# Kernel optimization log

Hardware: AMD Instinct MI355X
Metric: run time of the kernel (lower is better)

The kernel has to match this reference:

```python
import jax, jax.numpy as jnp
import numpy as np

DT = 0.02
Z_DIM = 32
U_DIM = 16


def _mlp(x, layers):
    # layers: list of (W, b); SiLU between all but last layer
    n = len(layers)
    for i, (W, b) in enumerate(layers):
        x = x @ W + b
        if i < n - 1:
            x = jax.nn.silu(x)
    return x


def _forward(x, u,
             e_w1, e_b1, e_w2, e_b2, e_w3, e_b3,
             d_w1, d_b1, d_w2, d_b2, d_w3, d_b3, d_w4, d_b4,
             a_w1, a_b1, a_w2, a_b2, a_w3, a_b3,
             b_w1, b_b1, b_w2, b_b2, b_w3, b_b3):
    # encode
    z = _mlp(x, [(e_w1, e_b1), (e_w2, e_b2), (e_w3, e_b3)])          # (B, Z)
    # state-dependent A(x) parameters: pairs (a_i, b_i) per 2x2 block
    aux = _mlp(x, [(a_w1, a_b1), (a_w2, a_b2), (a_w3, a_b3)])        # (B, Z)
    a = aux[:, 0::2]                                                  # (B, Z/2)
    b = aux[:, 1::2]
    f = jnp.exp(a * DT)
    c = jnp.cos(b * DT)
    s = jnp.sin(b * DT)
    # A(x) @ z without materializing block-diagonal: per-pair rotation-scale
    z0 = z[:, 0::2]
    z1 = z[:, 1::2]
    Az = jnp.stack([f * (c * z0 - s * z1), f * (s * z0 + c * z1)], axis=-1).reshape(z.shape)
    # B(x) @ u
    Bmat = _mlp(x, [(b_w1, b_b1), (b_w2, b_b2), (b_w3, b_b3)]).reshape(-1, Z_DIM, U_DIM)
    Bu = jnp.einsum('bzu,bu->bz', Bmat, u)
    # latent Euler step + decode
    z_next = z + DT * (Az + Bu)
    return _mlp(z_next, [(d_w1, d_b1), (d_w2, d_b2), (d_w3, d_b3), (d_w4, d_b4)])


def setup_inputs() -> dict:
    key = jax.random.key(0)
    ks = iter(jax.random.split(key, 32))
    def w(shape, scale=0.02):
        return jax.random.normal(next(ks), shape, jnp.float32) * scale
    B, X, U, Z, H, A = 16384, 64, 16, 32, 1024, 256
    return {
        'x': jax.random.normal(next(ks), (B, X), jnp.float32),
        'u': jax.random.normal(next(ks), (B, U), jnp.float32),
        'e_w1': w((X, H)), 'e_b1': w((H,)),
        'e_w2': w((H, H)), 'e_b2': w((H,)),
        'e_w3': w((H, Z)), 'e_b3': w((Z,)),
        'd_w1': w((Z, H)), 'd_b1': w((H,)),
        'd_w2': w((H, H)), 'd_b2': w((H,)),
        'd_w3': w((H, H)), 'd_b3': w((H,)),
        'd_w4': w((H, X)), 'd_b4': w((X,)),
        'a_w1': w((X, A)), 'a_b1': w((A,)),
        'a_w2': w((A, A)), 'a_b2': w((A,)),
        'a_w3': w((A, Z)), 'a_b3': w((Z,)),
        'b_w1': w((X, A)), 'b_b1': w((A,)),
        'b_w2': w((A, A)), 'b_b2': w((A,)),
        'b_w3': w((A, Z * U)), 'b_b3': w((Z * U,)),
    }


def reference(x, u,
              e_w1, e_b1, e_w2, e_b2, e_w3, e_b3,
              d_w1, d_b1, d_w2, d_b2, d_w3, d_b3, d_w4, d_b4,
              a_w1, a_b1, a_w2, a_b2, a_w3, a_b3,
              b_w1, b_b1, b_w2, b_b2, b_w3, b_b3):
    return _forward(x, u,
                    e_w1, e_b1, e_w2, e_b2, e_w3, e_b3,
                    d_w1, d_b1, d_w2, d_b2, d_w3, d_b3, d_w4, d_b4,
                    a_w1, a_b1, a_w2, a_b2, a_w3, a_b3,
                    b_w1, b_b1, b_w2, b_b2, b_w3, b_b3)
```

## Files before the change

kernel.cpp:

```cpp
#include <hip/hip_runtime.h>
#include <cstdint>
#include <cstddef>

#define B_SZ 16384
#define X_D  64
#define U_D  16
#define Z_D  32
#define H_D  1024
#define A_D  256
#define DT_C 0.02f

typedef _Float16 f16;
typedef f16   f16x8 __attribute__((ext_vector_type(8)));
typedef f16   f16x4 __attribute__((ext_vector_type(4)));
typedef float f32x4 __attribute__((ext_vector_type(4)));
typedef float f32x16 __attribute__((ext_vector_type(16)));

#define AS1 __attribute__((address_space(1)))
#define AS3 __attribute__((address_space(3)))

__device__ __forceinline__ void gld_lds16(const void* g, void* l) {
    __builtin_amdgcn_global_load_lds((AS1 void*)(g), (AS3 void*)(l), 16, 0, 0);
}

struct GArg {
    const f16*  A;
    const f16*  W;
    const float* bias;
    void*       C;
    int lda, ldc, K;
};
struct GSet { GArg g[3]; int yn0, yn1; };

template<int BM,int BN,int BK,int WM,int WN,bool SILU,int OM>
__launch_bounds__(256)
__global__ void gemm_k(GSet p)
{
    static_assert(OM != 1 || BN == 128, "OM1 repack assumes BN=128");
    int yb = blockIdx.y, gi = 0;
    if (yb >= p.yn0) { yb -= p.yn0; gi = 1; if (yb >= p.yn1) { yb -= p.yn1; gi = 2; } }
    const GArg ga = p.g[gi];

    constexpr int SEGROW = BK / 8;
    constexpr int SMASK  = (SEGROW < 8 ? SEGROW : 8) - 1;
    constexpr int WTM = BM / WM, WTN = BN / WN;
    static_assert(WTM % 32 == 0 && WTN % 32 == 0, "wave tile in 32x32 units");
    constexpr int RM = WTM / 32, RN = WTN / 32;
    constexpr int KS = BK / 16;
    constexpr int ITA = (BM * SEGROW) / 256;
    constexpr int ITB = (BN * SEGROW) / 256;

    constexpr int STAGE_B = (BM + BN) * BK * 2;
    constexpr int CS_B    = (OM == 1) ? BM * BN * 2 : 0;
    constexpr int SMEM_B  = STAGE_B > CS_B ? STAGE_B : CS_B;
    __shared__ __align__(16) char smem[SMEM_B];
    f16* As = (f16*)smem;
    f16* Bs = As + BM * BK;

    const int tid  = threadIdx.x;
    const int lane = tid & 63;
    const int wave = tid >> 6;
    const int wm = wave / WN, wn = wave % WN;
    const int l31 = lane & 31, half = lane >> 5;

    const size_t arow0 = (size_t)blockIdx.x * BM;
    const size_t brow0 = (size_t)yb * BN;
    const int lda = ga.lda, K = ga.K;

    const f16* aptr[ITA];
    const f16* bptr[ITB];
#pragma unroll
    for (int it = 0; it < ITA; ++it) {
        int s = it * 256 + tid;
        int row = s / SEGROW, st = s % SEGROW;
        int sg = st ^ (row & SMASK);
        aptr[it] = ga.A + (arow0 + row) * lda + sg * 8;
    }
#pragma unroll
    for (int it = 0; it < ITB; ++it) {
        int s = it * 256 + tid;
        int row = s / SEGROW, st = s % SEGROW;
        int sg = st ^ (row & SMASK);
        bptr[it] = ga.W + (brow0 + row) * K + sg * 8;
    }

    f32x16 acc[RM][RN];
#pragma unroll
    for (int i = 0; i < RM; ++i)
#pragma unroll
        for (int j = 0; j < RN; ++j)
#pragma unroll
            for (int r = 0; r < 16; ++r) acc[i][j][r] = 0.f;

    for (int k0 = 0; k0 < K; k0 += BK) {
#pragma unroll
        for (int it = 0; it < ITA; ++it) {
            gld_lds16(aptr[it], &As[(it * 256 + tid) * 8]);
            aptr[it] += BK;
        }
#pragma unroll
        for (int it = 0; it < ITB; ++it) {
            gld_lds16(bptr[it], &Bs[(it * 256 + tid) * 8]);
            bptr[it] += BK;
        }
        __syncthreads();

#pragma unroll
        for (int ks = 0; ks < KS; ++ks) {
            f16x8 af[RM], bf[RN];
#pragma unroll
            for (int i = 0; i < RM; ++i) {
                int row = wm * WTM + i * 32 + l31;
                int st  = (ks * 2 + half) ^ (row & SMASK);
                af[i] = *(const f16x8*)&As[(row * SEGROW + st) * 8];
            }
#pragma unroll
            for (int j = 0; j < RN; ++j) {
                int row = wn * WTN + j * 32 + l31;
                int st  = (ks * 2 + half) ^ (row & SMASK);
                bf[j] = *(const f16x8*)&Bs[(row * SEGROW + st) * 8];
            }
#pragma unroll
            for (int i = 0; i < RM; ++i)
#pragma unroll
                for (int j = 0; j < RN; ++j)
                    acc[i][j] = __builtin_amdgcn_mfma_f32_32x32x16_f16(
                        af[i], bf[j], acc[i][j], 0, 0, 0);
        }
        __syncthreads();
    }

    const int rowbL = wm * WTM;
    const int colbL = wn * WTN;

    if constexpr (OM == 1) {
        f16* Cs = (f16*)smem;
#pragma unroll
        for (int j = 0; j < RN; ++j) {
            int colL = colbL + j * 32 + l31;
            float bv = ga.bias[(int)brow0 + colL];
            int chL = colL >> 3, wi = colL & 7;
#pragma unroll
            for (int i = 0; i < RM; ++i) {
#pragma unroll
                for (int r = 0; r < 16; ++r) {
                    int rowL = rowbL + i * 32 + (r & 3) + 8 * (r >> 2) + 4 * half;
                    float v = acc[i][j][r] + bv;
                    if (SILU) v = v / (1.0f + __expf(-v));
                    Cs[rowL * BN + ((chL ^ (rowL & 15)) << 3) + wi] = (f16)v;
                }
            }
        }
        __syncthreads();
        f16* Cout = (f16*)ga.C;
#pragma unroll
        for (int pass = 0; pass < (BM * BN / 8) / 256; ++pass) {
            int s = pass * 256 + tid;
            int rowL = s >> 4;
            int ch = s & 15;
            f16x8 v = *(const f16x8*)&Cs[rowL * BN + ((ch ^ (rowL & 15)) << 3)];
            *(f16x8*)&Cout[(size_t)(arow0 + rowL) * ga.ldc + brow0 + ch * 8] = v;
        }
    } else {
        float* Cout = (float*)ga.C;
#pragma unroll
        for (int j = 0; j < RN; ++j) {
            int col = (int)brow0 + colbL + j * 32 + l31;
            float bv = ga.bias[col];
#pragma unroll
            for (int i = 0; i < RM; ++i) {
#pragma unroll
                for (int r = 0; r < 16; ++r) {
                    int row = (int)arow0 + rowbL + i * 32
                            + (r & 3) + 8 * (r >> 2) + 4 * half;
                    float v = acc[i][j][r] + bv;
                    if (SILU) v = v / (1.0f + __expf(-v));
                    Cout[(size_t)row * ga.ldc + col] = v;
                }
            }
        }
    }
}

__launch_bounds__(256)
__global__ void mid_k(const f16* __restrict__ cc2,
                      const f16* __restrict__ e_w3t, const float* __restrict__ e_b3,
                      const f16* __restrict__ a_w3t, const float* __restrict__ a_b3,
                      const f16* __restrict__ b_w3t, const float* __restrict__ b_b3,
                      const float* __restrict__ u,   f16* __restrict__ znb)
{
    __shared__ __align__(16) f16 As[32 * 64];
    __shared__ __align__(16) f16 Bs[128 * 64];
    __shared__ float zb[32 * 32];
    __shared__ float ab[32 * 32];
    __shared__ float bu[32 * 32];
    __shared__ float ub[32 * 16];

    const int tid  = threadIdx.x;
    const int lane = tid & 63, wave = tid >> 6;
    const int l15 = lane & 15, quad = lane >> 4;
    const int r0 = blockIdx.x * 32;

    ub[tid]       = u[r0 * 16 + tid];
    ub[tid + 256] = u[r0 * 16 + 256 + tid];

#pragma unroll 1
    for (int ph = 0; ph < 2; ++ph) {
        const f16* W    = ph ? a_w3t : e_w3t;
        const float* bs = ph ? a_b3 : e_b3;
        const int K     = ph ? 256 : 1024;
        const int co    = ph ? 1024 : 0;
        float* ob       = ph ? ab : zb;
        f32x4 acc = {0.f, 0.f, 0.f, 0.f};
        for (int k0 = 0; k0 < K; k0 += 64) {
            {
                int row = tid >> 3, sg = (tid & 7) ^ (row & 7);
                gld_lds16(cc2 + (size_t)(r0 + row) * 1536 + co + k0 + sg * 8,
                          &As[tid * 8]);
            }
            {
                int row = tid >> 3, sg = (tid & 7) ^ (row & 7);
                gld_lds16(W + (size_t)row * K + k0 + sg * 8, &Bs[tid * 8]);
            }
            __syncthreads();
#pragma unroll
            for (int kk = 0; kk < 64; kk += 32) {
                int ar = ((wave >> 1) << 4) + l15;
                int ast = ((kk >> 3) + quad) ^ (ar & 7);
                f16x8 af = *(const f16x8*)&As[(ar * 8 + ast) * 8];
                int br = ((wave & 1) << 4) + l15;
                int bst = ((kk >> 3) + quad) ^ (br & 7);
                f16x8 bf = *(const f16x8*)&Bs[(br * 8 + bst) * 8];
                acc = __builtin_amdgcn_mfma_f32_16x16x32_f16(af, bf, acc, 0, 0, 0);
            }
            __syncthreads();
        }
#pragma unroll
        for (int r = 0; r < 4; ++r) {
            int row = ((wave >> 1) << 4) + quad * 4 + r;
            int col = ((wave & 1) << 4) + l15;
            ob[row * 32 + col] = acc[r] + bs[col];
        }
    }

#pragma unroll 1
    for (int ch = 0; ch < 4; ++ch) {
        f32x4 acc[2][2];
#pragma unroll
        for (int i = 0; i < 2; ++i)
#pragma unroll
            for (int j = 0; j < 2; ++j) acc[i][j] = f32x4{0.f, 0.f, 0.f, 0.f};
        for (int k0 = 0; k0 < 256; k0 += 64) {
            {   int row = tid >> 3, sg = (tid & 7) ^ (row & 7);
                gld_lds16(cc2 + (size_t)(r0 + row) * 1536 + 1280 + k0 + sg * 8,
                          &As[tid * 8]);
            }
#pragma unroll
            for (int it = 0; it < 4; ++it) {
                int s = it * 256 + tid;
                int row = s >> 3, sg = (s & 7) ^ (row & 7);
                gld_lds16(b_w3t + (size_t)(ch * 128 + row) * 256 + k0 + sg * 8,
                          &Bs[s * 8]);
            }
            __syncthreads();
#pragma unroll
            for (int kk = 0; kk < 64; kk += 32) {
                f16x8 af[2], bf[2];
#pragma unroll
                for (int i = 0; i < 2; ++i) {
                    int ar = i * 16 + l15;
                    int st = ((kk >> 3) + quad) ^ (ar & 7);
                    af[i] = *(const f16x8*)&As[(ar * 8 + st) * 8];
                }
#pragma unroll
                for (int j = 0; j < 2; ++j) {
                    int br = wave * 32 + j * 16 + l15;
                    int st = ((kk >> 3) + quad) ^ (br & 7);
                    bf[j] = *(const f16x8*)&Bs[(br * 8 + st) * 8];
                }
#pragma unroll
                for (int i = 0; i < 2; ++i)
#pragma unroll
                    for (int j = 0; j < 2; ++j)
                        acc[i][j] = __builtin_amdgcn_mfma_f32_16x16x32_f16(
                            af[i], bf[j], acc[i][j], 0, 0, 0);
            }
            __syncthreads();
        }
#pragma unroll
        for (int j = 0; j < 2; ++j) {
            int colg = ch * 128 + wave * 32 + j * 16 + l15;
            float bv = b_b3[colg];
            int z = colg >> 4;
#pragma unroll
            for (int i = 0; i < 2; ++i) {
#pragma unroll
                for (int r = 0; r < 4; ++r) {
                    int row = i * 16 + quad * 4 + r;
                    float v = (acc[i][j][r] + bv) * ub[row * 16 + l15];
                    v += __shfl_xor(v, 8, 16);
                    v += __shfl_xor(v, 4, 16);
                    v += __shfl_xor(v, 2, 16);
                    v += __shfl_xor(v, 1, 16);
                    if (l15 == 0) bu[row * 32 + z] = v;
                }
            }
        }
    }
    __syncthreads();

#pragma unroll
    for (int t = 0; t < 4; ++t) {
        int idx = t * 256 + tid;
        int row = idx >> 5, z = idx & 31;
        int pb = idx & ~1;
        float a  = ab[pb], b = ab[pb + 1];
        float z0 = zb[pb], z1 = zb[pb + 1];
        float f  = __expf(a * DT_C);
        float c_ = __cosf(b * DT_C);
        float s_ = __sinf(b * DT_C);
        float Az = (z & 1) ? f * (s_ * z0 + c_ * z1) : f * (c_ * z0 - s_ * z1);
        float zc = (z & 1) ? z1 : z0;
        znb[(size_t)(r0 + row) * 32 + z] = (f16)(zc + DT_C * (Az + bu[idx]));
    }
}

struct PrepArgs {
    const float* w[13];
    f16*         wt[13];
    int          K[13];
    int          N[13];
    const float* bsrc[3];
    float*       bias1;
    const float* x;
    f16*         xb;
};

__launch_bounds__(256)
__global__ void prep_k(PrepArgs pa, int ntrans, int ncvt)
{
    int bid = blockIdx.x;
    if (bid < ntrans) {
        int i = 0, t;
        for (;; ++i) {
            t = (pa.K[i] >> 5) * (pa.N[i] >> 5);
            if (bid < t) break;
            bid -= t;
        }
        const int K = pa.K[i], N = pa.N[i];
        const int tn = N >> 5;
        const int k0 = (bid / tn) << 5, n0 = (bid % tn) << 5;
        __shared__ float tbuf[32][33];
        const int tx = threadIdx.x & 31, ty = threadIdx.x >> 5;
        const float* src = pa.w[i];
        f16* dst = pa.wt[i];
#pragma unroll
        for (int r = 0; r < 32; r += 8)
            tbuf[ty + r][tx] = src[(size_t)(k0 + ty + r) * N + n0 + tx];
        __syncthreads();
#pragma unroll
        for (int r = 0; r < 32; r += 8)
            dst[(size_t)(n0 + ty + r) * K + k0 + tx] = (f16)tbuf[tx][ty + r];
    } else if (bid < ntrans + ncvt) {
        int i = ((bid - ntrans) * 256 + threadIdx.x) * 4;
        float4 v = *(const float4*)(pa.x + i);
        f16x4 o = {(f16)v.x, (f16)v.y, (f16)v.z, (f16)v.w};
        *(f16x4*)(pa.xb + i) = o;
    } else {
        int idx = (bid - ntrans - ncvt) * 256 + (int)threadIdx.x;
        float v = (idx < 1024) ? pa.bsrc[0][idx]
                : (idx < 1280) ? pa.bsrc[1][idx - 1024]
                               : pa.bsrc[2][idx - 1280];
        pa.bias1[idx] = v;
    }
}

extern "C" void kernel_launch(void* const* d_in, const int* in_sizes, int n_in,
                              void* d_out, int out_size, void* d_ws, size_t ws_size,
                              hipStream_t stream)
{
    (void)in_sizes; (void)n_in; (void)out_size; (void)ws_size;
    const float* x    = (const float*)d_in[0];
    const float* u    = (const float*)d_in[1];
    const float* e_w1 = (const float*)d_in[2];  const float* e_b1 = (const float*)d_in[3];
    const float* e_w2 = (const float*)d_in[4];  const float* e_b2 = (const float*)d_in[5];
    const float* e_w3 = (const float*)d_in[6];  const float* e_b3 = (const float*)d_in[7];
    const float* d_w1 = (const float*)d_in[8];  const float* d_b1 = (const float*)d_in[9];
    const float* d_w2 = (const float*)d_in[10]; const float* d_b2 = (const float*)d_in[11];
    const float* d_w3 = (const float*)d_in[12]; const float* d_b3 = (const float*)d_in[13];
    const float* d_w4 = (const float*)d_in[14]; const float* d_b4 = (const float*)d_in[15];
    const float* a_w1 = (const float*)d_in[16]; const float* a_b1 = (const float*)d_in[17];
    const float* a_w2 = (const float*)d_in[18]; const float* a_b2 = (const float*)d_in[19];
    const float* a_w3 = (const float*)d_in[20]; const float* a_b3 = (const float*)d_in[21];
    const float* b_w1 = (const float*)d_in[22]; const float* b_b1 = (const float*)d_in[23];
    const float* b_w2 = (const float*)d_in[24]; const float* b_b2 = (const float*)d_in[25];
    const float* b_w3 = (const float*)d_in[26]; const float* b_b3 = (const float*)d_in[27];

    char* p = (char*)d_ws;
    auto alloc = [&](size_t nbytes) -> void* {
        void* r = (void*)p;
        p += (nbytes + 255) & ~(size_t)255;
        return r;
    };
    f16*   xb   = (f16*)  alloc((size_t)B_SZ * X_D * 2);
    f16*   cc1  = (f16*)  alloc((size_t)B_SZ * 1536 * 2);
    f16*   cc2  = (f16*)  alloc((size_t)B_SZ * 1536 * 2);
    f16*   znb  = (f16*)  alloc((size_t)B_SZ * Z_D * 2);
    f16*   h1d  = cc1;
    f16*   h2d  = cc2;
    f16*   h3d  = cc1;
    f16*   W1t   = (f16*)alloc((size_t)1536 * X_D * 2);
    float* bias1 = (float*)alloc(1536 * 4);
    f16* e_w2t = (f16*)alloc((size_t)H_D * H_D * 2);
    f16* e_w3t = (f16*)alloc((size_t)Z_D * H_D * 2);
    f16* d_w1t = (f16*)alloc((size_t)H_D * Z_D * 2);
    f16* d_w2t = (f16*)alloc((size_t)H_D * H_D * 2);
    f16* d_w3t = (f16*)alloc((size_t)H_D * H_D * 2);
    f16* d_w4t = (f16*)alloc((size_t)X_D * H_D * 2);
    f16* a_w2t = (f16*)alloc((size_t)A_D * A_D * 2);
    f16* a_w3t = (f16*)alloc((size_t)Z_D * A_D * 2);
    f16* b_w2t = (f16*)alloc((size_t)A_D * A_D * 2);
    f16* b_w3t = (f16*)alloc((size_t)(Z_D * U_D) * A_D * 2);

    PrepArgs pa;
    const float* ws_[13] = {e_w1, e_w2, e_w3, d_w1, d_w2, d_w3, d_w4,
                            a_w1, a_w2, a_w3, b_w1, b_w2, b_w3};
    f16* wts_[13] = {W1t, e_w2t, e_w3t, d_w1t, d_w2t, d_w3t, d_w4t,
                     W1t + (size_t)1024 * X_D, a_w2t, a_w3t,
                     W1t + (size_t)1280 * X_D, b_w2t, b_w3t};
    int Ks_[13] = {X_D, H_D, H_D, Z_D, H_D, H_D, H_D, X_D, A_D, A_D, X_D, A_D, A_D};
    int Ns_[13] = {H_D, H_D, Z_D, H_D, H_D, H_D, X_D, A_D, A_D, Z_D, A_D, A_D, Z_D*U_D};
    int ntrans = 0;
    for (int i = 0; i < 13; ++i) {
        pa.w[i] = ws_[i]; pa.wt[i] = wts_[i]; pa.K[i] = Ks_[i]; pa.N[i] = Ns_[i];
        ntrans += (Ks_[i] >> 5) * (Ns_[i] >> 5);
    }
    pa.bsrc[0] = e_b1; pa.bsrc[1] = a_b1; pa.bsrc[2] = b_b1;
    pa.bias1 = bias1; pa.x = x; pa.xb = xb;
    const int ncvt = (B_SZ * X_D) / 1024;
    prep_k<<<ntrans + ncvt + 6, 256, 0, stream>>>(pa, ntrans, ncvt);

    auto G = [](const f16* A, const f16* W, const float* bias, void* C,
                int lda, int ldc, int K) {
        GArg g; g.A = A; g.W = W; g.bias = bias; g.C = C;
        g.lda = lda; g.ldc = ldc; g.K = K; return g;
    };
    GSet s;

    s.g[0] = G(xb, W1t, bias1, cc1, X_D, 1536, X_D);
    s.yn0 = 12; s.yn1 = 0;
    gemm_k<128,128,64,2,2,true,1><<<dim3(B_SZ/128, 12), 256, 0, stream>>>(s);

    s.g[0] = G(cc1,        e_w2t, e_b2, cc2,        1536, 1536, H_D);
    s.g[1] = G(cc1 + 1024, a_w2t, a_b2, cc2 + 1024, 1536, 1536, A_D);
    s.g[2] = G(cc1 + 1280, b_w2t, b_b2, cc2 + 1280, 1536, 1536, A_D);
    s.yn0 = 8; s.yn1 = 2;
    gemm_k<128,128,64,2,2,true,1><<<dim3(B_SZ/128, 12), 256, 0, stream>>>(s);

    mid_k<<<B_SZ/32, 256, 0, stream>>>(cc2, e_w3t, e_b3, a_w3t, a_b3,
                                       b_w3t, b_b3, u, znb);

    s.yn0 = 8; s.yn1 = 0;
    s.g[0] = G(znb, d_w1t, d_b1, h1d, Z_D, H_D, Z_D);
    gemm_k<128,128,32,2,2,true,1><<<dim3(B_SZ/128, 8), 256, 0, stream>>>(s);

    s.g[0] = G(h1d, d_w2t, d_b2, h2d, H_D, H_D, H_D);
    gemm_k<128,128,64,2,2,true,1><<<dim3(B_SZ/128, 8), 256, 0, stream>>>(s);

    s.g[0] = G(h2d, d_w3t, d_b3, h3d, H_D, H_D, H_D);
    gemm_k<128,128,64,2,2,true,1><<<dim3(B_SZ/128, 8), 256, 0, stream>>>(s);

    s.g[0] = G(h3d, d_w4t, d_b4, d_out, H_D, X_D, H_D);
    s.yn0 = 1;
    gemm_k<64,64,64,2,2,false,0><<<dim3(B_SZ/64, 1), 256, 0, stream>>>(s);
}
```

Baseline: 368.2 us.

## Double-buffer LDS tiles in the GEMM kernel to overlap loads with MFMA

Splits shared memory into two staging buffers and restructures the K loop so the next tile's global-to-LDS loads are issued before computing on the current tile. One barrier per tile remains, instead of a barrier after the loads plus one after the compute. The aim is to hide global load latency behind MFMA work. In exchange, LDS use per block roughly doubles, which may lower occupancy.

```diff
diff --git a/kernel.cpp b/kernel.cpp
--- a/kernel.cpp
+++ b/kernel.cpp
@@ -50,12 +50,13 @@
     constexpr int ITA = (BM * SEGROW) / 256;
     constexpr int ITB = (BN * SEGROW) / 256;
 
-    constexpr int STAGE_B = (BM + BN) * BK * 2;
-    constexpr int CS_B    = (OM == 1) ? BM * BN * 2 : 0;
-    constexpr int SMEM_B  = STAGE_B > CS_B ? STAGE_B : CS_B;
-    __shared__ __align__(16) char smem[SMEM_B];
-    f16* As = (f16*)smem;
-    f16* Bs = As + BM * BK;
+    constexpr int HALF_B = (BM + BN) * BK * 2;
+    constexpr int CS_B   = (OM == 1) ? BM * BN * 2 : 0;
+    constexpr int S0_B   = HALF_B > CS_B ? HALF_B : CS_B;
+    __shared__ __align__(16) char smem0[S0_B];
+    __shared__ __align__(16) char smem1[HALF_B];
+    f16* As0 = (f16*)smem0;  f16* Bs0 = As0 + BM * BK;
+    f16* As1 = (f16*)smem1;  f16* Bs1 = As1 + BM * BK;
 
     const int tid  = threadIdx.x;
     const int lane = tid & 63;
@@ -92,7 +93,7 @@
 #pragma unroll
             for (int r = 0; r < 16; ++r) acc[i][j][r] = 0.f;
 
-    for (int k0 = 0; k0 < K; k0 += BK) {
+    auto stage = [&](f16* As, f16* Bs) {
 #pragma unroll
         for (int it = 0; it < ITA; ++it) {
             gld_lds16(aptr[it], &As[(it * 256 + tid) * 8]);
@@ -103,8 +104,9 @@
             gld_lds16(bptr[it], &Bs[(it * 256 + tid) * 8]);
             bptr[it] += BK;
         }
-        __syncthreads();
-
+    };
+
+    auto compute = [&](const f16* As, const f16* Bs) {
 #pragma unroll
         for (int ks = 0; ks < KS; ++ks) {
             f16x8 af[RM], bf[RN];
@@ -127,14 +129,32 @@
                     acc[i][j] = __builtin_amdgcn_mfma_f32_32x32x16_f16(
                         af[i], bf[j], acc[i][j], 0, 0, 0);
         }
+    };
+
+    const int nt = K / BK;
+    stage(As0, Bs0);
+    __syncthreads();
+    if (nt == 1) {
+        compute(As0, Bs0);
         __syncthreads();
+    } else {
+        for (int t = 0; t < nt; t += 2) {
+            if (t + 1 < nt) stage(As1, Bs1);
+            compute(As0, Bs0);
+            __syncthreads();
+            if (t + 2 < nt) stage(As0, Bs0);
+            if (t + 1 < nt) {
+                compute(As1, Bs1);
+                __syncthreads();
+            }
+        }
     }
 
     const int rowbL = wm * WTM;
     const int colbL = wn * WTN;
 
     if constexpr (OM == 1) {
-        f16* Cs = (f16*)smem;
+        f16* Cs = (f16*)smem0;
 #pragma unroll
         for (int j = 0; j < RN; ++j) {
             int colL = colbL + j * 32 + l31;
```

New measurement: 450.0 us. 1.22x slower.

## Add 256x256-tile 8-wave pipelined GEMM kernel for the large hidden layers

Applied to the files above, without the earlier changes.

Adds a new GEMM kernel with 512 threads and a 256x256 output tile, used for the big hidden-layer GEMMs (encoder and aux layer 2, decoder layers 2 and 3). It double-buffers K slices in 128KB of LDS via direct global-to-LDS loads and uses an XOR-swizzled layout with explicit barriers and waitcnts. It raises wave priority around the MFMA bursts and writes the output through a swizzled LDS staging buffer for coalesced f16 stores. The larger tile is meant to cut global and LDS traffic per flop and overlap loads with compute. The risks are fewer blocks (384 or 256 on a 256-CU part), tail imbalance, and occupancy limited by the large LDS footprint.

```diff
diff --git a/kernel.cpp b/kernel.cpp
--- a/kernel.cpp
+++ b/kernel.cpp
@@ -22,6 +22,13 @@
 __device__ __forceinline__ void gld_lds16(const void* g, void* l) {
     __builtin_amdgcn_global_load_lds((AS1 void*)(g), (AS3 void*)(l), 16, 0, 0);
 }
+
+#define BARX()  do { asm volatile("" ::: "memory"); __builtin_amdgcn_s_barrier(); \
+                     asm volatile("" ::: "memory"); } while (0)
+#define LGK0()  do { asm volatile("s_waitcnt lgkmcnt(0)" ::: "memory"); \
+                     __builtin_amdgcn_sched_barrier(0); } while (0)
+#define WAITV4() asm volatile("s_waitcnt vmcnt(4)" ::: "memory")
+#define WAITV0() asm volatile("s_waitcnt vmcnt(0)" ::: "memory")
 
 struct GArg {
     const f16*  A;
@@ -179,6 +186,150 @@
                 }
             }
         }
+    }
+}
+
+template<bool SILU>
+__launch_bounds__(512, 2)
+__global__ void gemm8_k(GSet p)
+{
+    int yb = blockIdx.y, gi = 0;
+    if (yb >= p.yn0) { yb -= p.yn0; gi = 1; if (yb >= p.yn1) { yb -= p.yn1; gi = 2; } }
+    const GArg ga = p.g[gi];
+
+    __shared__ __align__(16) char smem[131072];
+
+    const int tid  = threadIdx.x;
+    const int lane = tid & 63, wave = tid >> 6;
+    const int wm = wave >> 2, wn = wave & 3;
+    const int l31 = lane & 31, half = lane >> 5;
+
+    const size_t arow0 = (size_t)blockIdx.x * 256;
+    const size_t brow0 = (size_t)yb * 256;
+    const int lda = ga.lda, K = ga.K;
+    const int nt = K >> 6;
+
+    const f16* sp[4][2];
+#pragma unroll
+    for (int q = 0; q < 2; ++q) {
+        int ls = q * 512 + tid;
+        int r  = ls >> 2;
+        int lseg = (ls & 3) ^ ((r >> 1) & 3);
+        sp[0][q] = ga.A + (arow0 + r) * lda +      lseg * 8;
+        sp[2][q] = ga.A + (arow0 + r) * lda + 32 + lseg * 8;
+        sp[1][q] = ga.W + (brow0 + r) * K   +      lseg * 8;
+        sp[3][q] = ga.W + (brow0 + r) * K   + 32 + lseg * 8;
+    }
+
+    f32x16 acc[4][2];
+#pragma unroll
+    for (int i = 0; i < 4; ++i)
+#pragma unroll
+        for (int j = 0; j < 2; ++j)
+#pragma unroll
+            for (int r = 0; r < 16; ++r) acc[i][j][r] = 0.f;
+
+    f16x8 af[2][2];
+    f16x8 bf[2][2];
+
+    auto stage_u = [&](int u, int bb) {
+        char* base = smem + ((u & 1) ? 65536 : 0) + (size_t)(bb * 2 + (u >> 1)) * 16384;
+        gld_lds16(sp[u][0], base + (size_t)tid * 16);         sp[u][0] += 64;
+        gld_lds16(sp[u][1], base + (size_t)(512 + tid) * 16); sp[u][1] += 64;
+    };
+    auto readA = [&](int b, int kp, int mh) {
+#pragma unroll
+        for (int m2 = 0; m2 < 2; ++m2)
+#pragma unroll
+            for (int ks = 0; ks < 2; ++ks) {
+                int row = wm * 128 + (mh * 2 + m2) * 32 + l31;
+                int ps  = (ks * 2 + half) ^ ((row >> 1) & 3);
+                af[m2][ks] = *(const f16x8*)(smem
+                    + (size_t)(b * 2 + kp) * 16384 + row * 64 + ps * 16);
+            }
+    };
+    auto readB = [&](int b, int kp) {
+#pragma unroll
+        for (int nf = 0; nf < 2; ++nf)
+#pragma unroll
+            for (int ks = 0; ks < 2; ++ks) {
+                int row = wn * 64 + nf * 32 + l31;
+                int ps  = (ks * 2 + half) ^ ((row >> 1) & 3);
+                bf[nf][ks] = *(const f16x8*)(smem + 65536
+                    + (size_t)(b * 2 + kp) * 16384 + row * 64 + ps * 16);
+            }
+    };
+    auto mma = [&](int mh) {
+        __builtin_amdgcn_s_setprio(1);
+#pragma unroll
+        for (int ks = 0; ks < 2; ++ks)
+#pragma unroll
+            for (int m2 = 0; m2 < 2; ++m2)
+#pragma unroll
+                for (int nf = 0; nf < 2; ++nf)
+                    acc[mh * 2 + m2][nf] = __builtin_amdgcn_mfma_f32_32x32x16_f16(
+                        af[m2][ks], bf[nf][ks], acc[mh * 2 + m2][nf], 0, 0, 0);
+        __builtin_amdgcn_s_setprio(0);
+    };
+
+    auto tile = [&](int b, bool dostage) {
+        readA(b, 0, 0); readB(b, 0);
+        if (dostage) stage_u(0, b ^ 1);
+        BARX(); LGK0();
+        mma(0);
+        BARX();
+        readA(b, 0, 1);
+        if (dostage) stage_u(1, b ^ 1);
+        BARX(); LGK0();
+        mma(1);
+        if (dostage) WAITV4(); else WAITV0();
+        BARX();
+        readA(b, 1, 0); readB(b, 1);
+        if (dostage) stage_u(2, b ^ 1);
+        BARX(); LGK0();
+        mma(0);
+        BARX();
+        readA(b, 1, 1);
+        if (dostage) stage_u(3, b ^ 1);
+        BARX(); LGK0();
+        mma(1);
+        if (dostage) WAITV4();
+        BARX();
+    };
+
+    stage_u(0, 0); stage_u(1, 0); stage_u(2, 0); stage_u(3, 0);
+    WAITV4();
+    BARX();
+
+    int t = 0;
+    for (; t + 2 < nt; t += 2) { tile(0, true); tile(1, true); }
+    tile(0, true);
+    tile(1, false);
+
+    f16* Cs = (f16*)smem;
+#pragma unroll
+    for (int mf = 0; mf < 4; ++mf)
+#pragma unroll
+        for (int nf = 0; nf < 2; ++nf) {
+            int colL = wn * 64 + nf * 32 + l31;
+            float bv = ga.bias[(int)brow0 + colL];
+            int ch = colL >> 3, wi = colL & 7;
+#pragma unroll
+            for (int r = 0; r < 16; ++r) {
+                int rowL = wm * 128 + mf * 32 + (r & 3) + 8 * (r >> 2) + 4 * half;
+                float v = acc[mf][nf][r] + bv;
+                if (SILU) v = v / (1.0f + __expf(-v));
+                Cs[rowL * 256 + ((ch ^ (rowL & 31)) << 3) + wi] = (f16)v;
+            }
+        }
+    __syncthreads();
+    f16* Cout = (f16*)ga.C;
+#pragma unroll
+    for (int pass = 0; pass < 16; ++pass) {
+        int s = pass * 512 + tid;
+        int rowL = s >> 5, ch = s & 31;
+        f16x8 v = *(const f16x8*)&Cs[rowL * 256 + ((ch ^ (rowL & 31)) << 3)];
+        *(f16x8*)&Cout[(size_t)(arow0 + rowL) * ga.ldc + brow0 + ch * 8] = v;
     }
 }
 
@@ -454,8 +605,8 @@
     s.g[0] = G(cc1,        e_w2t, e_b2, cc2,        1536, 1536, H_D);
     s.g[1] = G(cc1 + 1024, a_w2t, a_b2, cc2 + 1024, 1536, 1536, A_D);
     s.g[2] = G(cc1 + 1280, b_w2t, b_b2, cc2 + 1280, 1536, 1536, A_D);
-    s.yn0 = 8; s.yn1 = 2;
-    gemm_k<128,128,64,2,2,true,1><<<dim3(B_SZ/128, 12), 256, 0, stream>>>(s);
+    s.yn0 = 4; s.yn1 = 1;
+    gemm8_k<true><<<dim3(B_SZ/256, 6), 512, 0, stream>>>(s);
 
     mid_k<<<B_SZ/32, 256, 0, stream>>>(cc2, e_w3t, e_b3, a_w3t, a_b3,
                                        b_w3t, b_b3, u, znb);
@@ -464,11 +615,12 @@
     s.g[0] = G(znb, d_w1t, d_b1, h1d, Z_D, H_D, Z_D);
     gemm_k<128,128,32,2,2,true,1><<<dim3(B_SZ/128, 8), 256, 0, stream>>>(s);
 
+    s.yn0 = 4; s.yn1 = 0;
     s.g[0] = G(h1d, d_w2t, d_b2, h2d, H_D, H_D, H_D);
-    gemm_k<128,128,64,2,2,true,1><<<dim3(B_SZ/128, 8), 256, 0, stream>>>(s);
+    gemm8_k<true><<<dim3(B_SZ/256, 4), 512, 0, stream>>>(s);
 
     s.g[0] = G(h2d, d_w3t, d_b3, h3d, H_D, H_D, H_D);
-    gemm_k<128,128,64,2,2,true,1><<<dim3(B_SZ/128, 8), 256, 0, stream>>>(s);
+    gemm8_k<true><<<dim3(B_SZ/256, 4), 512, 0, stream>>>(s);
 
     s.g[0] = G(h3d, d_w4t, d_b4, d_out, H_D, X_D, H_D);
     s.yn0 = 1;
```

Result: no change. 371.8 us (+1.0%).
